# Optimization experiments

Measured on AMD Instinct MI355X. Metric: run time of the kernel, lower is better.

## Reference

```python
import math
import jax, jax.numpy as jnp
import numpy as np


def _precompute_psi(nlat_in, nlon_in, nlat_out, K, theta_cutoff):
    """Faithful numpy port of _precompute_convolution_tensor (equiangular grids).
    Returns COO indices (k, t, lat_in, lon_in) and float values of the sparse
    filter tensor psi of logical shape [K, nlat_out, nlat_in*nlon_in]."""
    lats_in = np.linspace(0.0, np.pi, nlat_in)
    lats_out = np.linspace(0.0, np.pi, nlat_out)
    phis = np.linspace(-np.pi, np.pi, nlon_in)
    d_theta = theta_cutoff / K
    theta_i = np.arange(K) * d_theta  # (K,)
    ks, ts, las, los, vs = [], [], [], [], []
    alpha = -lats_in[:, None]          # (nlat_in, 1)
    beta = phis[None, :]               # (1, nlon_in)
    for t in range(nlat_out):
        gamma = lats_out[t]
        z = np.cos(alpha) * np.cos(gamma) - np.cos(beta) * np.sin(alpha) * np.sin(gamma)
        theta = np.arccos(np.clip(z, -1.0, 1.0))   # (nlat_in, nlon_in)
        diff = np.abs(theta[None, :, :] - theta_i[:, None, None])  # (K, nlat_in, nlon_in)
        mask = (diff < d_theta) & (theta[None, :, :] < theta_cutoff)
        k_idx, la_idx, lo_idx = np.nonzero(mask)
        v = 1.0 - diff[k_idx, la_idx, lo_idx] / d_theta  # triangle (hat) weights
        ks.append(k_idx); ts.append(np.full_like(k_idx, t)); las.append(la_idx); los.append(lo_idx); vs.append(v)
    return (np.concatenate(ks).astype(np.int32),
            np.concatenate(ts).astype(np.int32),
            np.concatenate(las).astype(np.int32),
            np.concatenate(los).astype(np.int32),
            np.concatenate(vs).astype(np.float32))


def setup_inputs() -> dict:
    B, C = 4, 32
    nlat_in, nlon_in = 361, 720
    nlat_out, nlon_out = 361, 720
    K = 3
    theta_cutoff = 0.01 * math.pi  # default used at the precompute call site
    k, t, la, lo, v = _precompute_psi(nlat_in, nlon_in, nlat_out, K, theta_cutoff)
    key = jax.random.key(0)
    x = jax.random.normal(key, (B, C, nlat_in, nlon_in), dtype=jnp.float32)
    return {
        "x": x,
        "psi_vals": jnp.asarray(v),
        "psi_k": jnp.asarray(k),
        "psi_t": jnp.asarray(t),
        "psi_lat": jnp.asarray(la),
        "psi_lon": jnp.asarray(lo),
        "kernel_size": K,
        "nlat_out": nlat_out,
        "nlon_out": nlon_out,
    }


def reference(x, psi_vals, psi_k, psi_t, psi_lat, psi_lon, kernel_size, nlat_out, nlon_out):
    B, C, nlat_in, nlon_in = x.shape
    BC = B * C
    scale = nlon_in // nlon_out  # = 1 here
    # (nlat_in, nlon_in, BC) layout, matching x.reshape(B*C,...).permute(1,2,0)
    xr = x.reshape(BC, nlat_in, nlon_in).transpose(1, 2, 0)
    seg = psi_k * nlat_out + psi_t           # row id in the (K*nlat_out) output
    num_seg = kernel_size * nlat_out

    def step(_, p):
        # torch.roll(x, scale, dims=lon) applied (p+1) times before the bmm:
        # rolled[lat, lon] = x[lat, (lon - (p+1)*scale) % nlon]
        lon_idx = (psi_lon - (p + 1) * scale) % nlon_in
        g = xr[psi_lat, lon_idx]             # (nnz, BC) irregular gather
        out_p = jax.ops.segment_sum(psi_vals[:, None] * g, seg, num_segments=num_seg)
        return None, out_p                   # (K*nlat_out, BC)

    _, outs = jax.lax.scan(step, None, jnp.arange(nlon_out))  # (nlon_out, K*nlat_out, BC)
    outs = outs.reshape(nlon_out, kernel_size, nlat_out, BC)
    # permute(3,1,2,0) then split BC -> (B, C)
    return outs.transpose(3, 1, 2, 0).reshape(B, C, kernel_size, nlat_out, nlon_out)
```

## Files before the change

### kernel.cpp

```cpp
#include <hip/hip_runtime.h>
#include <math.h>


#define NLAT 361
#define NLON 720
#define KK 3
#define PTILE 80
#define NPX 9
#define NT 320
#define PD 88
#define SWN 896
#define TOTCAP (720*1024)

typedef __attribute__((ext_vector_type(8))) short bf16x8;
typedef __attribute__((ext_vector_type(4))) float f32x4;
typedef __attribute__((ext_vector_type(4))) unsigned int u32x4;

#define D_PI 3.14159265358979311599796346854418516159057617187500
#define STEP_LAT (D_PI / 360.0)
#define STEP_PHI ((2.0 * D_PI) / 719.0)
#define CUTOFF (0.01 * D_PI)
#define DTH (CUTOFF / 3.0)

__device__ inline unsigned int bf16pair_rne(float lo, float hi) {
    unsigned int a = __builtin_bit_cast(unsigned int, lo);
    unsigned int b = __builtin_bit_cast(unsigned int, hi);
    a = a + 0x7fffu + ((a >> 16) & 1u);
    b = b + 0x7fffu + ((b >> 16) & 1u);
    return (a >> 16) | (b & 0xffff0000u);
}

__global__ __launch_bounds__(512) void bounds_kernel(int4* __restrict__ params,
                                                     float2* __restrict__ pAB,
                                                     unsigned long long* __restrict__ actd) {
    __shared__ int part[512];
    int tid = threadIdx.x;
    int rmins[9], Ws[9], bl8s[9];
    float As[9], Bs[9];
    int wsum = 0;
    if (tid < NLAT) {
        int t = tid;
        double g = (t == 360) ? D_PI : (double)t * STEP_LAT;
        double cg = cos(g), sg = sin(g);
        const double coscut = cos(CUTOFF);
#pragma unroll
        for (int d = 0; d < 9; ++d) {
            int la = t + d - 4;
            int rmin = 0, W = 0;
            double A = 0.0, Bc = 0.0;
            if (la >= 0 && la <= 360) {
                double lad = (la == 360) ? D_PI : (double)la * STEP_LAT;
                A = cos(lad) * cg;
                Bc = sin(lad) * sg;
                if (Bc < 1e-14) {
                    if (A > coscut) { rmin = 0; W = 720; }
                } else {
                    double C = (coscut - A) / Bc;
                    if (C <= -1.0) { rmin = 0; W = 720; }
                    else if (C < 1.0) {
                        double bmax = acos(C);
                        int r0 = (int)floor((D_PI - bmax) / STEP_PHI) + 1;
                        int r1 = (int)ceil((D_PI + bmax) / STEP_PHI) - 1;
                        if (r0 < 0) r0 = 0;
                        if (r1 > 719) r1 = 719;
                        rmin = r0; W = r1 - r0 + 1;
                        if (W < 0) W = 0;
                    }
                }
            }
            rmins[d] = rmin; Ws[d] = W;
            As[d] = (float)A; Bs[d] = (float)Bc;
            int b8 = 0;
            if (W > 0) {
                b8 = (W + 175) & ~7;
                if (b8 > SWN) b8 = SWN;
            }
            bl8s[d] = b8;
            wsum += b8;
        }
    }
    part[tid] = wsum;
    __syncthreads();
    for (int dd = 1; dd < 512; dd <<= 1) {
        int v = part[tid];
        int w2 = (tid >= dd) ? part[tid - dd] : 0;
        __syncthreads();
        part[tid] = v + w2;
        __syncthreads();
    }
    int base = part[tid] - wsum;
    if (tid < NLAT) {
        unsigned long long pk = 0;
        int nact = 0;
#pragma unroll
        for (int d = 0; d < 9; ++d) {
            int off = base;
            base += bl8s[d];
            if (Ws[d] > 0 && off + bl8s[d] <= TOTCAP) {
                params[tid * 9 + d] = make_int4(rmins[d], Ws[d], off, bl8s[d]);
                pAB[tid * 9 + d] = make_float2(As[d], Bs[d]);
                pk |= ((unsigned long long)d) << (4 + 4 * nact);
                nact++;
            } else {
                params[tid * 9 + d] = make_int4(0, 0, 0, 0);
            }
        }
        pk |= (unsigned long long)nact;
        actd[tid] = pk;
    }
}

__global__ __launch_bounds__(128) void fill_w_kernel(const int4* __restrict__ params,
                                                     const float2* __restrict__ pAB,
                                                     unsigned int* __restrict__ wtab) {
    int row = blockIdx.x;
    int4 pr = params[row];
    int W = pr.y;
    if (W <= 0) return;
    int rmin = pr.x, off = pr.z, bl8 = pr.w;
    float2 ab = pAB[row];
    float A = ab.x, Bc = ab.y;
    const float invd = (float)(1.0 / DTH);
    for (int idx = threadIdx.x; idx < bl8; idx += 128) {
        int j = idx - PD;
        float f1 = 1.0e9f, f2 = 1.0e9f;
        if (j >= 0 && j < W) {
            int lo = rmin + j;
            float beta = (lo == 719) ? (float)D_PI : (float)((double)lo * STEP_PHI - D_PI);
            float z = fminf(1.f, fmaxf(-1.f, fmaf(Bc, cosf(beta), A)));
            f1 = acosf(z) * invd;
        }
        if (j + 1 >= 0 && j + 1 < W) {
            int lo = rmin + j + 1;
            float beta = (lo == 719) ? (float)D_PI : (float)((double)lo * STEP_PHI - D_PI);
            float z = fminf(1.f, fmaxf(-1.f, fmaf(Bc, cosf(beta), A)));
            f2 = acosf(z) * invd;
        }
        float w0a = fmaxf(0.f, 1.f - f1);
        float w1a = fmaxf(0.f, 1.f - fabsf(f1 - 1.f));
        float w2a = fmaxf(0.f, 1.f - fabsf(f1 - 2.f));
        float w0b = fmaxf(0.f, 1.f - f2);
        float w1b = fmaxf(0.f, 1.f - fabsf(f2 - 1.f));
        float w2b = fmaxf(0.f, 1.f - fabsf(f2 - 2.f));
        wtab[0 * TOTCAP + off + idx] = bf16pair_rne(w0a, w0b);
        wtab[1 * TOTCAP + off + idx] = bf16pair_rne(w1a, w1b);
        wtab[2 * TOTCAP + off + idx] = bf16pair_rne(w2a, w2b);
    }
}

__global__ void cvt_x_kernel(const float* __restrict__ x, unsigned int* __restrict__ xb,
                             int n8) {
    for (int i = blockIdx.x * 256 + threadIdx.x; i < n8; i += gridDim.x * 256) {
        f32x4 a = __builtin_nontemporal_load((const f32x4*)(x + (size_t)i * 8));
        f32x4 b = __builtin_nontemporal_load((const f32x4*)(x + (size_t)i * 8 + 4));
        u32x4 q;
        q.x = bf16pair_rne(a.x, a.y);
        q.y = bf16pair_rne(a.z, a.w);
        q.z = bf16pair_rne(b.x, b.y);
        q.w = bf16pair_rne(b.z, b.w);
        *(u32x4*)(xb + (size_t)i * 4) = q;
    }
}

template <int USEBF16>
__global__ __launch_bounds__(NT, 2) void dconv_mfma_kernel(
    const float* __restrict__ x, const unsigned short* __restrict__ xb,
    const int4* __restrict__ params, const unsigned long long* __restrict__ actd,
    const unsigned int* __restrict__ wtab, float* __restrict__ out) {
    __shared__ __attribute__((aligned(16))) unsigned char sB[128 * 128];
    __shared__ unsigned int sWi[KK * SWN];

    int bid = blockIdx.x;
    int r = bid & 7;
    int rest = bid >> 3;
    int px = rest % 9;
    int q = rest / 9;
    int yp = 8 * q + r;
    if (yp > 360) return;
    int t = (yp & 1) ? (360 - (yp >> 1)) : (yp >> 1);
    int p0 = px * PTILE;
    int tid = threadIdx.x;
    int lane = tid & 63;
    int psub = tid >> 6;
    int l15 = lane & 15;
    int l4 = lane >> 4;

    f32x4 acc[8][KK];
#pragma unroll
    for (int n = 0; n < 8; ++n)
#pragma unroll
        for (int k = 0; k < KK; ++k) acc[n][k] = (f32x4){0.f, 0.f, 0.f, 0.f};

    unsigned long long pk = actd[t];
    int nact = (int)(pk & 15ull);

    int c = 0, iact = 0;
    int la = 0, W = 0, off = 0, bl8 = 0, mbase = 0, shift = 0;
    int nK = 0, nC = 1, ks_lo = 0, ks_hi = -1;

    unsigned int wra[3], wrb[3], wrc[3];
    u32x4 br[4];

    auto LOADP = [&](int dd) {
        la = t + dd - 4;
        int4 pr = params[t * 9 + dd];
        int rmin = pr.x;
        W = pr.y; off = pr.z; bl8 = pr.w;
        int ms0 = rmin - PTILE - p0;
        shift = (ms0 + 720) & 7;
        nK = (W + 79 + shift + 31) >> 5;
        nC = (nK + 1) >> 1;
        mbase = (((ms0 - shift) % 720) + 720) % 720;
        int s_off = psub * 16 + 9 - shift;
        int kl = (73 - s_off) >> 5;
        ks_lo = kl < 0 ? 0 : kl;
        int kh = (87 + W - s_off) >> 5;
        ks_hi = kh > nK - 1 ? nK - 1 : kh;
    };
    auto ISSUE_W = [&]() {
#pragma unroll
        for (int pass = 0; pass < 3; ++pass) {
            int idx = pass * NT + tid;
            bool g2 = idx < bl8;
            wra[pass] = g2 ? wtab[0 * TOTCAP + off + idx] : 0u;
            wrb[pass] = g2 ? wtab[1 * TOTCAP + off + idx] : 0u;
            wrc[pass] = g2 ? wtab[2 * TOTCAP + off + idx] : 0u;
        }
    };
    auto WRITE_W = [&]() {
#pragma unroll
        for (int pass = 0; pass < 3; ++pass) {
            int idx = pass * NT + tid;
            if (idx < bl8) {
                sWi[0 * SWN + idx] = wra[pass];
                sWi[1 * SWN + idx] = wrb[pass];
                sWi[2 * SWN + idx] = wrc[pass];
            }
        }
    };
    auto ISSUE_B = [&](int cc) {
#pragma unroll
        for (int pass = 0; pass < 4; ++pass) {
            int slot = pass * NT + tid;
            if (slot < 1024) {
                int bc = slot >> 3;
                int mo = (slot & 7) * 8;
                int mg = mbase + cc * 64 + mo;
                mg -= (mg >= 720) ? 720 : 0;
                mg -= (mg >= 720) ? 720 : 0;
                mg -= (mg >= 720) ? 720 : 0;
                if (USEBF16) {
                    br[pass] = *(const u32x4*)(xb + ((size_t)bc * NLAT + la) * NLON + mg);
                } else {
                    const float* src = x + ((size_t)bc * NLAT + la) * NLON + mg;
                    f32x4 a = *(const f32x4*)(src);
                    f32x4 b = *(const f32x4*)(src + 4);
                    u32x4 qq;
                    qq.x = bf16pair_rne(a.x, a.y);
                    qq.y = bf16pair_rne(a.z, a.w);
                    qq.z = bf16pair_rne(b.x, b.y);
                    qq.w = bf16pair_rne(b.z, b.w);
                    br[pass] = qq;
                }
            }
        }
    };
    auto WRITE_B = [&]() {
#pragma unroll
        for (int pass = 0; pass < 4; ++pass) {
            int slot = pass * NT + tid;
            if (slot < 1024) {
                int bc = slot >> 3;
                int mo = (slot & 7) * 8;
                int cw = (mo * 2) ^ ((bc & 7) << 4);
                *(u32x4*)(sB + bc * 128 + cw) = br[pass];
            }
        }
    };

    LOADP((int)((pk >> 4) & 15ull));
    ISSUE_W();
    ISSUE_B(0);

    while (true) {
        __syncthreads();
        if (c == 0) WRITE_W();
        WRITE_B();
        __syncthreads();
        int shiftS = shift;
        int c2 = c * 2;
        int kloS = ks_lo > c2 ? ks_lo : c2;
        int khiS = ks_hi < c2 + 1 ? ks_hi : c2 + 1;
        bool done = false;
        if (c + 1 < nC) {
            c = c + 1;
            ISSUE_B(c);
        } else if (iact + 1 < nact) {
            iact++;
            c = 0;
            LOADP((int)((pk >> (4 + 4 * iact)) & 15ull));
            ISSUE_W();
            ISSUE_B(0);
        } else {
            done = true;
        }
        int soffS = psub * 16 + 9 - shiftS;
        for (int ks = kloS; ks <= khiS; ++ks) {
            int ksl = ks - c2;
            int s = ks * 32 + l4 * 8 + soffS + l15;
            bf16x8 af[KK];
#pragma unroll
            for (int k = 0; k < KK; ++k) {
                const unsigned int* wp = sWi + k * SWN + s;
                u32x4 qf;
                qf.x = wp[0];
                qf.y = wp[2];
                qf.z = wp[4];
                qf.w = wp[6];
                af[k] = __builtin_bit_cast(bf16x8, qf);
            }
            int colbase = ksl * 64 + l4 * 16;
#pragma unroll
            for (int n = 0; n < 8; ++n) {
                int brow = n * 16 + l15;
                int colb = colbase ^ ((brow & 7) << 4);
                bf16x8 bfv = *(const bf16x8*)(sB + brow * 128 + colb);
                acc[n][0] = __builtin_amdgcn_mfma_f32_16x16x32_bf16(af[0], bfv, acc[n][0], 0, 0, 0);
                acc[n][1] = __builtin_amdgcn_mfma_f32_16x16x32_bf16(af[1], bfv, acc[n][1], 0, 0, 0);
                acc[n][2] = __builtin_amdgcn_mfma_f32_16x16x32_bf16(af[2], bfv, acc[n][2], 0, 0, 0);
            }
        }
        if (done) break;
    }

    int p = p0 + psub * 16 + l4 * 4;
#pragma unroll
    for (int n = 0; n < 8; ++n) {
        int bc = n * 16 + l15;
#pragma unroll
        for (int k = 0; k < KK; ++k) {
            float* o = out + (((size_t)bc * KK + k) * NLAT + t) * NLON + p;
            __builtin_nontemporal_store(acc[n][k], (f32x4*)o);
        }
    }
}

extern "C" void kernel_launch(void* const* d_in, const int* in_sizes, int n_in,
                              void* d_out, int out_size, void* d_ws, size_t ws_size,
                              hipStream_t stream) {
    const float* x = (const float*)d_in[0];
    float* out = (float*)d_out;

    char* ws = (char*)d_ws;
    int4* params = (int4*)(ws + 0);
    float2* pAB = (float2*)(ws + 53248);
    unsigned long long* actd = (unsigned long long*)(ws + 81920);
    unsigned int* wtab = (unsigned int*)(ws + 90112);
    size_t xb_off = (90112 + (size_t)3 * TOTCAP * 4 + 4095) & ~(size_t)4095;
    size_t xb_bytes = (size_t)128 * NLAT * NLON * 2;
    int use_bf16 = (ws_size >= xb_off + xb_bytes) ? 1 : 0;
    unsigned short* xb = (unsigned short*)(ws + xb_off);

    bounds_kernel<<<1, 512, 0, stream>>>(params, pAB, actd);
    fill_w_kernel<<<NLAT * 9, 128, 0, stream>>>(params, pAB, wtab);

    dim3 grid(8 * NPX * 46, 1, 1);
    if (use_bf16) {
        int n8 = 128 * NLAT * NLON / 8;
        cvt_x_kernel<<<2048, 256, 0, stream>>>(x, (unsigned int*)xb, n8);
        dconv_mfma_kernel<1><<<grid, NT, 0, stream>>>(x, xb, params, actd, wtab, out);
    } else {
        dconv_mfma_kernel<0><<<grid, NT, 0, stream>>>(x, xb, params, actd, wtab, out);
    }
}
```

Before: 345.8 us.

## Double-buffer LDS via direct global-to-LDS loads, smaller pixel tiles, split BC across waves

Replaces the register-staged global→LDS copies with global_load_lds direct loads into double-buffered B and weight tiles, so the next chunk's fetch overlaps the current chunk's MFMA work and one barrier per iteration goes away. The pixel tile shrinks from 80 to 48 and each wave pair splits the 128 BC columns, which halves accumulators per wave and targets 4 blocks per CU. It also drops the nontemporal loads and stores. The cost is more halo overlap per tile (more redundant x reads), and the host launch grid must match the new NPX.

```diff
diff --git a/kernel.cpp b/kernel.cpp
--- a/kernel.cpp
+++ b/kernel.cpp
@@ -5,11 +5,11 @@
 #define NLAT 361
 #define NLON 720
 #define KK 3
-#define PTILE 80
-#define NPX 9
-#define NT 320
-#define PD 88
-#define SWN 896
+#define PTILE 48
+#define NPX 15
+#define NT 384
+#define PD 56
+#define SWN 832
 #define TOTCAP (720*1024)
 
 typedef __attribute__((ext_vector_type(8))) short bf16x8;
@@ -21,6 +21,17 @@
 #define STEP_PHI ((2.0 * D_PI) / 719.0)
 #define CUTOFF (0.01 * D_PI)
 #define DTH (CUTOFF / 3.0)
+
+__device__ __forceinline__ void gll16(const void* g, void* l) {
+    __builtin_amdgcn_global_load_lds(
+        (const __attribute__((address_space(1))) void*)g,
+        (__attribute__((address_space(3))) void*)l, 16, 0, 0);
+}
+__device__ __forceinline__ void gll4(const void* g, void* l) {
+    __builtin_amdgcn_global_load_lds(
+        (const __attribute__((address_space(1))) void*)g,
+        (__attribute__((address_space(3))) void*)l, 4, 0, 0);
+}
 
 __device__ inline unsigned int bf16pair_rne(float lo, float hi) {
     unsigned int a = __builtin_bit_cast(unsigned int, lo);
@@ -72,7 +83,7 @@
             As[d] = (float)A; Bs[d] = (float)Bc;
             int b8 = 0;
             if (W > 0) {
-                b8 = (W + 175) & ~7;
+                b8 = (W + 111) & ~7;
                 if (b8 > SWN) b8 = SWN;
             }
             bl8s[d] = b8;
@@ -151,8 +162,8 @@
 __global__ void cvt_x_kernel(const float* __restrict__ x, unsigned int* __restrict__ xb,
                              int n8) {
     for (int i = blockIdx.x * 256 + threadIdx.x; i < n8; i += gridDim.x * 256) {
-        f32x4 a = __builtin_nontemporal_load((const f32x4*)(x + (size_t)i * 8));
-        f32x4 b = __builtin_nontemporal_load((const f32x4*)(x + (size_t)i * 8 + 4));
+        f32x4 a = *(const f32x4*)(x + (size_t)i * 8);
+        f32x4 b = *(const f32x4*)(x + (size_t)i * 8 + 4);
         u32x4 q;
         q.x = bf16pair_rne(a.x, a.y);
         q.y = bf16pair_rne(a.z, a.w);
@@ -163,31 +174,33 @@
 }
 
 template <int USEBF16>
-__global__ __launch_bounds__(NT, 2) void dconv_mfma_kernel(
+__global__ __launch_bounds__(NT, 4) void dconv_mfma_kernel(
     const float* __restrict__ x, const unsigned short* __restrict__ xb,
     const int4* __restrict__ params, const unsigned long long* __restrict__ actd,
     const unsigned int* __restrict__ wtab, float* __restrict__ out) {
-    __shared__ __attribute__((aligned(16))) unsigned char sB[128 * 128];
-    __shared__ unsigned int sWi[KK * SWN];
+    __shared__ __attribute__((aligned(16))) unsigned char sB[2][128 * 128];
+    __shared__ unsigned int sWi[2][KK * SWN];
 
     int bid = blockIdx.x;
     int r = bid & 7;
     int rest = bid >> 3;
-    int px = rest % 9;
-    int q = rest / 9;
+    int px = rest % NPX;
+    int q = rest / NPX;
     int yp = 8 * q + r;
     if (yp > 360) return;
     int t = (yp & 1) ? (360 - (yp >> 1)) : (yp >> 1);
     int p0 = px * PTILE;
     int tid = threadIdx.x;
     int lane = tid & 63;
-    int psub = tid >> 6;
+    int w = tid >> 6;
+    int psub = w >> 1;
+    int bc0w = (w & 1) * 64;
     int l15 = lane & 15;
     int l4 = lane >> 4;
 
-    f32x4 acc[8][KK];
-#pragma unroll
-    for (int n = 0; n < 8; ++n)
+    f32x4 acc[4][KK];
+#pragma unroll
+    for (int n = 0; n < 4; ++n)
 #pragma unroll
         for (int k = 0; k < KK; ++k) acc[n][k] = (f32x4){0.f, 0.f, 0.f, 0.f};
 
@@ -197,60 +210,39 @@
     int c = 0, iact = 0;
     int la = 0, W = 0, off = 0, bl8 = 0, mbase = 0, shift = 0;
     int nK = 0, nC = 1, ks_lo = 0, ks_hi = -1;
-
-    unsigned int wra[3], wrb[3], wrc[3];
-    u32x4 br[4];
 
     auto LOADP = [&](int dd) {
         la = t + dd - 4;
         int4 pr = params[t * 9 + dd];
         int rmin = pr.x;
         W = pr.y; off = pr.z; bl8 = pr.w;
-        int ms0 = rmin - PTILE - p0;
+        int ms0 = rmin - 48 - p0;
         shift = (ms0 + 720) & 7;
-        nK = (W + 79 + shift + 31) >> 5;
+        nK = (W + 47 + shift + 31) >> 5;
         nC = (nK + 1) >> 1;
         mbase = (((ms0 - shift) % 720) + 720) % 720;
         int s_off = psub * 16 + 9 - shift;
-        int kl = (73 - s_off) >> 5;
+        int kl = (9 - s_off + 31) >> 5;
         ks_lo = kl < 0 ? 0 : kl;
-        int kh = (87 + W - s_off) >> 5;
+        int kh = (55 + W - s_off) >> 5;
         ks_hi = kh > nK - 1 ? nK - 1 : kh;
     };
-    auto ISSUE_W = [&]() {
+
+    auto ISSUE = [&](int cc, bool rowstart, int pbuf, int rbuf) {
 #pragma unroll
         for (int pass = 0; pass < 3; ++pass) {
-            int idx = pass * NT + tid;
-            bool g2 = idx < bl8;
-            wra[pass] = g2 ? wtab[0 * TOTCAP + off + idx] : 0u;
-            wrb[pass] = g2 ? wtab[1 * TOTCAP + off + idx] : 0u;
-            wrc[pass] = g2 ? wtab[2 * TOTCAP + off + idx] : 0u;
-        }
-    };
-    auto WRITE_W = [&]() {
-#pragma unroll
-        for (int pass = 0; pass < 3; ++pass) {
-            int idx = pass * NT + tid;
-            if (idx < bl8) {
-                sWi[0 * SWN + idx] = wra[pass];
-                sWi[1 * SWN + idx] = wrb[pass];
-                sWi[2 * SWN + idx] = wrc[pass];
-            }
-        }
-    };
-    auto ISSUE_B = [&](int cc) {
-#pragma unroll
-        for (int pass = 0; pass < 4; ++pass) {
             int slot = pass * NT + tid;
             if (slot < 1024) {
                 int bc = slot >> 3;
-                int mo = (slot & 7) * 8;
-                int mg = mbase + cc * 64 + mo;
+                int g = slot & 7;
+                int gs = g ^ (bc & 7);
+                int mg = mbase + cc * 64 + gs * 8;
                 mg -= (mg >= 720) ? 720 : 0;
                 mg -= (mg >= 720) ? 720 : 0;
                 mg -= (mg >= 720) ? 720 : 0;
                 if (USEBF16) {
-                    br[pass] = *(const u32x4*)(xb + ((size_t)bc * NLAT + la) * NLON + mg);
+                    gll16(xb + ((size_t)bc * NLAT + la) * NLON + mg,
+                          &sB[pbuf][slot * 16]);
                 } else {
                     const float* src = x + ((size_t)bc * NLAT + la) * NLON + mg;
                     f32x4 a = *(const f32x4*)(src);
@@ -260,49 +252,56 @@
                     qq.y = bf16pair_rne(a.z, a.w);
                     qq.z = bf16pair_rne(b.x, b.y);
                     qq.w = bf16pair_rne(b.z, b.w);
-                    br[pass] = qq;
+                    *(u32x4*)(&sB[pbuf][slot * 16]) = qq;
                 }
             }
         }
+        if (rowstart) {
+#pragma unroll
+            for (int pass = 0; pass < 3; ++pass) {
+                int idx = pass * NT + tid;
+                if (idx < bl8) {
+                    if (USEBF16) {
+                        gll4(wtab + 0 * TOTCAP + off + idx, &sWi[rbuf][0 * SWN + idx]);
+                        gll4(wtab + 1 * TOTCAP + off + idx, &sWi[rbuf][1 * SWN + idx]);
+                        gll4(wtab + 2 * TOTCAP + off + idx, &sWi[rbuf][2 * SWN + idx]);
+                    } else {
+                        sWi[rbuf][0 * SWN + idx] = wtab[0 * TOTCAP + off + idx];
+                        sWi[rbuf][1 * SWN + idx] = wtab[1 * TOTCAP + off + idx];
+                        sWi[rbuf][2 * SWN + idx] = wtab[2 * TOTCAP + off + idx];
+                    }
+                }
+            }
+        }
     };
-    auto WRITE_B = [&]() {
-#pragma unroll
-        for (int pass = 0; pass < 4; ++pass) {
-            int slot = pass * NT + tid;
-            if (slot < 1024) {
-                int bc = slot >> 3;
-                int mo = (slot & 7) * 8;
-                int cw = (mo * 2) ^ ((bc & 7) << 4);
-                *(u32x4*)(sB + bc * 128 + cw) = br[pass];
-            }
-        }
-    };
 
     LOADP((int)((pk >> 4) & 15ull));
-    ISSUE_W();
-    ISSUE_B(0);
+    ISSUE(0, true, 0, 0);
+    int pb = 0, rw = 0;
 
     while (true) {
-        __syncthreads();
-        if (c == 0) WRITE_W();
-        WRITE_B();
-        __syncthreads();
         int shiftS = shift;
         int c2 = c * 2;
         int kloS = ks_lo > c2 ? ks_lo : c2;
         int khiS = ks_hi < c2 + 1 ? ks_hi : c2 + 1;
-        bool done = false;
+        int pbC = pb, rwC = rw;
+        bool done = false, nrow = false;
         if (c + 1 < nC) {
             c = c + 1;
-            ISSUE_B(c);
         } else if (iact + 1 < nact) {
             iact++;
             c = 0;
             LOADP((int)((pk >> (4 + 4 * iact)) & 15ull));
-            ISSUE_W();
-            ISSUE_B(0);
+            nrow = true;
         } else {
             done = true;
+        }
+        if (USEBF16) asm volatile("s_waitcnt vmcnt(0)" ::: "memory");
+        __syncthreads();
+        if (!done) {
+            pb ^= 1;
+            if (nrow) rw ^= 1;
+            ISSUE(c, nrow, pb, rw);
         }
         int soffS = psub * 16 + 9 - shiftS;
         for (int ks = kloS; ks <= khiS; ++ks) {
@@ -311,7 +310,7 @@
             bf16x8 af[KK];
 #pragma unroll
             for (int k = 0; k < KK; ++k) {
-                const unsigned int* wp = sWi + k * SWN + s;
+                const unsigned int* wp = &sWi[rwC][k * SWN + s];
                 u32x4 qf;
                 qf.x = wp[0];
                 qf.y = wp[2];
@@ -321,10 +320,10 @@
             }
             int colbase = ksl * 64 + l4 * 16;
 #pragma unroll
-            for (int n = 0; n < 8; ++n) {
-                int brow = n * 16 + l15;
+            for (int n = 0; n < 4; ++n) {
+                int brow = bc0w + n * 16 + l15;
                 int colb = colbase ^ ((brow & 7) << 4);
-                bf16x8 bfv = *(const bf16x8*)(sB + brow * 128 + colb);
+                bf16x8 bfv = *(const bf16x8*)(&sB[pbC][brow * 128 + colb]);
                 acc[n][0] = __builtin_amdgcn_mfma_f32_16x16x32_bf16(af[0], bfv, acc[n][0], 0, 0, 0);
                 acc[n][1] = __builtin_amdgcn_mfma_f32_16x16x32_bf16(af[1], bfv, acc[n][1], 0, 0, 0);
                 acc[n][2] = __builtin_amdgcn_mfma_f32_16x16x32_bf16(af[2], bfv, acc[n][2], 0, 0, 0);
@@ -335,12 +334,12 @@
 
     int p = p0 + psub * 16 + l4 * 4;
 #pragma unroll
-    for (int n = 0; n < 8; ++n) {
-        int bc = n * 16 + l15;
+    for (int n = 0; n < 4; ++n) {
+        int bc = bc0w + n * 16 + l15;
 #pragma unroll
         for (int k = 0; k < KK; ++k) {
             float* o = out + (((size_t)bc * KK + k) * NLAT + t) * NLON + p;
-            __builtin_nontemporal_store(acc[n][k], (f32x4*)o);
+            *(f32x4*)o = acc[n][k];
         }
     }
 }
```

Result: faster. 292.4 us (-15.4%).
